# Kernel optimization log

Measured on AMD Instinct MI355X. Metric: run time of the kernel, lower is better.

The kernel has to match this reference:

```python
import jax, jax.numpy as jnp
import numpy as np

H = 256  # LSTM units == embedding dim

def _lstm(x, W, U, b):
    """Keras LSTM, return_sequences=True. x: [B,T,E] -> [B,T,H].
    Gate order i, f, g(c), o; sigmoid recurrent activation, tanh activation."""
    B = x.shape[0]
    xW = jnp.einsum('bte,eg->btg', x, W) + b  # [B,T,4H], input projection hoisted out of scan
    def step(carry, xw_t):
        h, c = carry
        z = xw_t + h @ U                      # [B,4H]
        i, f, g, o = jnp.split(z, 4, axis=-1)
        i = jax.nn.sigmoid(i); f = jax.nn.sigmoid(f)
        g = jnp.tanh(g);       o = jax.nn.sigmoid(o)
        c = f * c + i * g
        h = o * jnp.tanh(c)
        return (h, c), h
    h0 = jnp.zeros((B, H), x.dtype)
    (_, _), hs = jax.lax.scan(step, (h0, h0), jnp.swapaxes(xW, 0, 1))
    return jnp.swapaxes(hs, 0, 1)             # [B,T,H]

def _bilstm(x, Wf, Uf, bf, Wb, Ub, bb):
    fwd = _lstm(x, Wf, Uf, bf)
    bwd = _lstm(x[:, ::-1, :], Wb, Ub, bb)[:, ::-1, :]
    return jnp.concatenate([fwd, bwd], axis=-1)  # [B,T,2H]

def setup_inputs() -> dict:
    key = jax.random.key(0)
    ks = jax.random.split(key, 8)
    B, T, V, E = 256, 128, 32000, 256
    s = 0.05
    return {
        'tokens': jax.random.randint(ks[0], (B, T), 0, V, dtype=jnp.int32),
        'Emb': jax.random.normal(ks[1], (V, E), jnp.float32) * s,
        'Wf': jax.random.normal(ks[2], (3, E, 4 * H), jnp.float32) * s,
        'Uf': jax.random.normal(ks[3], (3, H, 4 * H), jnp.float32) * s,
        'bf': jnp.zeros((3, 4 * H), jnp.float32),
        'Wb': jax.random.normal(ks[4], (3, E, 4 * H), jnp.float32) * s,
        'Ub': jax.random.normal(ks[5], (3, H, 4 * H), jnp.float32) * s,
        'bb': jnp.zeros((3, 4 * H), jnp.float32),
    }

def reference(tokens, Emb, Wf, Uf, bf, Wb, Ub, bb):
    x = Emb[tokens]                             # [B,T,E]
    pools = []
    for l in range(3):                          # three parallel BiLSTM branches
        seq = _bilstm(x, Wf[l], Uf[l], bf[l], Wb[l], Ub[l], bb[l])  # [B,T,2H]
        pools.append(jnp.max(seq, axis=1))      # GlobalMaxPool1D -> [B,2H]
    return jnp.concatenate(pools, axis=1)       # [B,6H]
```

## Files before the change

### kernel.cpp

```cpp
#include <hip/hip_runtime.h>
#include <hip/hip_bf16.h>


#define NB 256
#define NT 128
#define NE 256
#define NH 256
#define NG 1024

using bf16x8 = __attribute__((ext_vector_type(8))) short;
using f32x4  = __attribute__((ext_vector_type(4))) float;
typedef unsigned long long u64;

#define X_OFF   0u
#define WT_OFF  16777216u
#define UT_OFF  19922944u
#define HB_OFF  23068672u
#define TAG_OFF 26214400u
#define HB_PAR_U64 196608

static __device__ __forceinline__ ushort f2bf(float f) {
  union { float f; unsigned u; } v; v.f = f;
  unsigned r = v.u + 0x7fffu + ((v.u >> 16) & 1u);
  return (ushort)(r >> 16);
}
static __device__ __forceinline__ float rcp_(float x) { return __builtin_amdgcn_rcpf(x); }
static __device__ __forceinline__ float sigf(float x) { return rcp_(1.f + __expf(-x)); }
static __device__ __forceinline__ float tanhf_(float x) { return 1.f - 2.f * rcp_(__expf(2.f * x) + 1.f); }

__global__ void k_embed(const int* __restrict__ tok, const float* __restrict__ emb,
                        ushort* __restrict__ x2) {
  const int tid = blockIdx.x * 256 + threadIdx.x;
  const int lane = tid & 63;
  const int nt = (tid >> 6) & 3;
  const int kt = (tid >> 8) & 7;
  const int bg = (tid >> 11) & 3;
  const int t  = tid >> 13;
  const int b  = bg * 64 + nt * 16 + (lane & 15);
  const int e0 = kt * 32 + (lane >> 4) * 8;
  const int tk = tok[b * NT + t];
  const float4 v0 = *(const float4*)(emb + (size_t)tk * NE + e0);
  const float4 v1 = *(const float4*)(emb + (size_t)tk * NE + e0 + 4);
  ushort4 o0, o1;
  o0.x = f2bf(v0.x); o0.y = f2bf(v0.y); o0.z = f2bf(v0.z); o0.w = f2bf(v0.w);
  o1.x = f2bf(v1.x); o1.y = f2bf(v1.y); o1.z = f2bf(v1.z); o1.w = f2bf(v1.w);
  ushort4* dst = (ushort4*)(x2 + (size_t)tid * 8);
  dst[0] = o0; dst[1] = o1;
}

__global__ void k_pack(const float* __restrict__ Wf, const float* __restrict__ Uf,
                       const float* __restrict__ Wb, const float* __restrict__ Ub,
                       ushort* __restrict__ wt, ushort* __restrict__ ut) {
  const int tid = blockIdx.x * 256 + threadIdx.x;
  const int l = tid & 63;
  const int mt = (tid >> 6) & 7;
  const int kt = (tid >> 9) & 7;
  const int cg = (tid >> 12) & 7;
  const int chain = tid >> 15;
  const int ll = chain >> 1, dir = chain & 1;
  const int ml = mt * 16 + (l & 15);
  const int hdl = ml >> 2, g = ml & 3;
  const int col = g * 256 + cg * 32 + hdl;
  const int k0 = kt * 32 + ((l >> 4) << 3);
  const float* W = (dir ? Wb : Wf) + (size_t)ll * NE * NG;
  const float* U = (dir ? Ub : Uf) + (size_t)ll * NH * NG;
  ushort vw[8], vu[8];
#pragma unroll
  for (int j = 0; j < 8; ++j) {
    vw[j] = f2bf(W[(size_t)(k0 + j) * NG + col]);
    vu[j] = f2bf(U[(size_t)(k0 + j) * NG + col]);
  }
  ushort4* dw = (ushort4*)(wt + (size_t)tid * 8);
  dw[0] = make_ushort4(vw[0], vw[1], vw[2], vw[3]);
  dw[1] = make_ushort4(vw[4], vw[5], vw[6], vw[7]);
  ushort4* du = (ushort4*)(ut + (size_t)tid * 8);
  du[0] = make_ushort4(vu[0], vu[1], vu[2], vu[3]);
  du[1] = make_ushort4(vu[4], vu[5], vu[6], vu[7]);
}

__global__ void k_init(uint* __restrict__ p) { p[threadIdx.x] = 0u; }

__global__ __launch_bounds__(512, 2) void k_lstm(
    const ushort* __restrict__ x2, const ushort* __restrict__ wt,
    const ushort* __restrict__ ut, const float* __restrict__ bf_,
    const float* __restrict__ bb_, ushort* __restrict__ hbuf,
    uint* __restrict__ tags, float* __restrict__ out) {
  __shared__ __align__(16) char smem[73728];

  const int bid = blockIdx.x;
  const int w = (bid & 7) * 24 + (bid >> 3);
  const int cg = w & 7, grp = w >> 3;
  const int chain = grp >> 2, bg = grp & 3;
  const int ll = chain >> 1, dir = chain & 1;
  const int tx = threadIdx.x;
  const int wv = tx >> 6, lane = tx & 63;
  const int mh = wv & 1, nt = wv >> 1;
  const int l15 = lane & 15, hi = lane >> 4;

  {
    const bf16x8* wsrc = (const bf16x8*)(wt + (size_t)(chain * 8 + cg) * 32768);
    bf16x8* wdst = (bf16x8*)smem;
#pragma unroll
    for (int i = 0; i < 8; ++i) wdst[i * 512 + tx] = wsrc[i * 512 + tx];
  }
  bf16x8 uf[8][4];
#pragma unroll
  for (int kt = 0; kt < 8; ++kt)
#pragma unroll
    for (int q = 0; q < 4; ++q)
      uf[kt][q] = *(const bf16x8*)(ut + ((size_t)((chain * 8 + cg) * 8 + kt) * 8 + mh * 4 + q) * 512 + lane * 8);

  const float* bias = (dir ? bb_ : bf_) + ll * NG;
  float bias_r[4][4];
#pragma unroll
  for (int q = 0; q < 4; ++q)
#pragma unroll
    for (int r = 0; r < 4; ++r)
      bias_r[q][r] = bias[r * 256 + cg * 32 + mh * 16 + q * 4 + hi];

  int pubaddr[4];
#pragma unroll
  for (int q = 0; q < 4; ++q) {
    const int lane2 = l15 | ((mh * 2 + (q >> 1)) << 4);
    const int slot = (q & 1) * 4 + hi;
    pubaddr[q] = 65536 + nt * 1024 + lane2 * 16 + slot * 2;
  }

  float c_[4] = {0.f, 0.f, 0.f, 0.f};
  float hm[4] = {-1e30f, -1e30f, -1e30f, -1e30f};

  uint* tag_own = tags + grp * 16 + cg;
  const uint* tag_poll = tags + grp * 16 + (lane & 7);
  u64* hb64 = (u64*)hbuf;
  __syncthreads();

  for (int tau = 0; tau < NT; ++tau) {
    const int t = dir ? (NT - 1 - tau) : tau;
    const ushort* xb_base = x2 + ((size_t)((t * 4 + bg) * 32 + nt)) * 512 + lane * 8;
    bf16x8 xb[8];
#pragma unroll
    for (int kt = 0; kt < 8; ++kt) xb[kt] = *(const bf16x8*)(xb_base + kt * 2048);

    f32x4 acc[4];
#pragma unroll
    for (int q = 0; q < 4; ++q)
      acc[q] = (f32x4){bias_r[q][0], bias_r[q][1], bias_r[q][2], bias_r[q][3]};

#pragma unroll
    for (int kt = 0; kt < 4; ++kt)
#pragma unroll
      for (int q = 0; q < 4; ++q) {
        const bf16x8 wA = *(const bf16x8*)(smem + ((kt * 8 + mh * 4 + q) * 64 + lane) * 16);
        acc[q] = __builtin_amdgcn_mfma_f32_16x16x32_bf16(wA, xb[kt], acc[q], 0, 0, 0);
      }

    if (tau > 0) {
      while (!__all(__hip_atomic_load(tag_poll, __ATOMIC_RELAXED, __HIP_MEMORY_SCOPE_AGENT) >= (uint)tau))
        __builtin_amdgcn_s_sleep(1);
      asm volatile("" ::: "memory");
    }

    u64 hq[16];
    if (tau > 0) {
      const u64* hs = hb64 + (size_t)((tau - 1) & 1) * HB_PAR_U64 + grp * 4096;
#pragma unroll
      for (int kt = 0; kt < 8; ++kt) {
        const int o = (kt * 4 + nt) * 128 + lane * 2;
        hq[kt * 2]     = __hip_atomic_load(hs + o,     __ATOMIC_RELAXED, __HIP_MEMORY_SCOPE_AGENT);
        hq[kt * 2 + 1] = __hip_atomic_load(hs + o + 1, __ATOMIC_RELAXED, __HIP_MEMORY_SCOPE_AGENT);
      }
    }

#pragma unroll
    for (int kt = 4; kt < 8; ++kt)
#pragma unroll
      for (int q = 0; q < 4; ++q) {
        const bf16x8 wA = *(const bf16x8*)(smem + ((kt * 8 + mh * 4 + q) * 64 + lane) * 16);
        acc[q] = __builtin_amdgcn_mfma_f32_16x16x32_bf16(wA, xb[kt], acc[q], 0, 0, 0);
      }

    if (tau > 0) {
#pragma unroll
      for (int kt = 0; kt < 8; ++kt) {
        union { u64 q[2]; bf16x8 v; } u;
        u.q[0] = hq[kt * 2]; u.q[1] = hq[kt * 2 + 1];
#pragma unroll
        for (int q = 0; q < 4; ++q)
          acc[q] = __builtin_amdgcn_mfma_f32_16x16x32_bf16(uf[kt][q], u.v, acc[q], 0, 0, 0);
      }
    }

    const int parb = (tau & 1) * 4096;
#pragma unroll
    for (int q = 0; q < 4; ++q) {
      const float iv = sigf(acc[q][0]);
      const float fv = sigf(acc[q][1]);
      const float gv = tanhf_(acc[q][2]);
      const float ov = sigf(acc[q][3]);
      const float cn = fv * c_[q] + iv * gv;
      c_[q] = cn;
      const float hv = ov * tanhf_(cn);
      hm[q] = fmaxf(hm[q], hv);
      *(ushort*)(smem + pubaddr[q] + parb) = f2bf(hv);
    }
    __syncthreads();

    if (tau + 1 < NT) {
      const u64 v = *(const u64*)(smem + 65536 + parb + tx * 8);
      __hip_atomic_store(hb64 + (size_t)(tau & 1) * HB_PAR_U64 + grp * 4096 + cg * 512 + tx,
                         v, __ATOMIC_RELAXED, __HIP_MEMORY_SCOPE_AGENT);
      asm volatile("s_waitcnt vmcnt(0)" ::: "memory");
      if (tx == 0)
        __hip_atomic_store(tag_own, (uint)(tau + 1), __ATOMIC_RELAXED, __HIP_MEMORY_SCOPE_AGENT);
    }
  }

#pragma unroll
  for (int q = 0; q < 4; ++q) {
    const int b = bg * 64 + nt * 16 + l15;
    const int col = ll * 512 + dir * 256 + cg * 32 + mh * 16 + q * 4 + hi;
    out[(size_t)b * 1536 + col] = hm[q];
  }
}

extern "C" void kernel_launch(void* const* d_in, const int* in_sizes, int n_in,
                              void* d_out, int out_size, void* d_ws, size_t ws_size,
                              hipStream_t stream) {
  (void)in_sizes; (void)n_in; (void)out_size; (void)ws_size;
  const int*   tokens = (const int*)d_in[0];
  const float* Emb    = (const float*)d_in[1];
  const float* Wf     = (const float*)d_in[2];
  const float* Uf     = (const float*)d_in[3];
  const float* bf_    = (const float*)d_in[4];
  const float* Wb     = (const float*)d_in[5];
  const float* Ub     = (const float*)d_in[6];
  const float* bb_    = (const float*)d_in[7];
  float* out = (float*)d_out;

  ushort* x2   = (ushort*)((char*)d_ws + X_OFF);
  ushort* wt   = (ushort*)((char*)d_ws + WT_OFF);
  ushort* ut   = (ushort*)((char*)d_ws + UT_OFF);
  ushort* hbuf = (ushort*)((char*)d_ws + HB_OFF);
  uint*   tags = (uint*)((char*)d_ws + TAG_OFF);

  hipLaunchKernelGGL(k_embed, dim3(4096), dim3(256), 0, stream, tokens, Emb, x2);
  hipLaunchKernelGGL(k_pack, dim3(768), dim3(256), 0, stream, Wf, Uf, Wb, Ub, wt, ut);
  hipLaunchKernelGGL(k_init, dim3(1), dim3(768), 0, stream, tags);
  hipLaunchKernelGGL(k_lstm, dim3(192), dim3(512), 0, stream, x2, wt, ut, bf_, bb_, hbuf, tags, out);
}
```

Measured before the change: 449.2 us.

## Pair forward and backward directions per block and pipeline hidden-state loads

Each block now runs both directions of one layer's column slice, with four waves per direction. Every wave covers all four batch tiles for two gate quads, so the grid halves to 96 blocks and each block holds both W slices in LDS. Hidden-state publishing now goes straight to global memory from each wave with per-wave tags, dropping the block-wide barrier and the LDS staging step. Polling is done by one wave per direction, which forwards readiness to the other waves through an LDS flag. The h loads are split into three batches interleaved with MFMAs to hide latency. In exchange, each block uses much more LDS and more registers, and the per-step publish now issues many scattered 2-byte atomic stores.

```diff
diff --git a/kernel.cpp b/kernel.cpp
--- a/kernel.cpp
+++ b/kernel.cpp
@@ -16,8 +16,9 @@
 #define WT_OFF  16777216u
 #define UT_OFF  19922944u
 #define HB_OFF  23068672u
-#define TAG_OFF 26214400u
-#define HB_PAR_U64 196608
+#define TAG_OFF 24641536u
+#define HB_PAR_U64 98304
+#define HB_PAR_US  393216
 
 static __device__ __forceinline__ ushort f2bf(float f) {
   union { float f; unsigned u; } v; v.f = f;
@@ -85,142 +86,208 @@
     const ushort* __restrict__ ut, const float* __restrict__ bf_,
     const float* __restrict__ bb_, ushort* __restrict__ hbuf,
     uint* __restrict__ tags, float* __restrict__ out) {
-  __shared__ __align__(16) char smem[73728];
+  __shared__ __align__(16) char smem[131200];
 
   const int bid = blockIdx.x;
-  const int w = (bid & 7) * 24 + (bid >> 3);
-  const int cg = w & 7, grp = w >> 3;
-  const int chain = grp >> 2, bg = grp & 3;
-  const int ll = chain >> 1, dir = chain & 1;
+  const int w = (bid & 7) * 12 + (bid >> 3);
+  const int ll = w >> 5, rr_ = w & 31, cg = rr_ >> 2, bg = rr_ & 3;
   const int tx = threadIdx.x;
   const int wv = tx >> 6, lane = tx & 63;
-  const int mh = wv & 1, nt = wv >> 1;
+  const int dir = wv >> 2, mq = wv & 3;
+  const int chain = ll * 2 + dir;
   const int l15 = lane & 15, hi = lane >> 4;
 
-  {
-    const bf16x8* wsrc = (const bf16x8*)(wt + (size_t)(chain * 8 + cg) * 32768);
-    bf16x8* wdst = (bf16x8*)smem;
+#pragma unroll
+  for (int d2 = 0; d2 < 2; ++d2) {
+    const bf16x8* wsrc = (const bf16x8*)(wt + (size_t)((ll * 2 + d2) * 8 + cg) * 32768);
+    bf16x8* wdst = (bf16x8*)(smem + d2 * 65536);
 #pragma unroll
     for (int i = 0; i < 8; ++i) wdst[i * 512 + tx] = wsrc[i * 512 + tx];
   }
-  bf16x8 uf[8][4];
+  bf16x8 uf[8][2];
 #pragma unroll
   for (int kt = 0; kt < 8; ++kt)
 #pragma unroll
-    for (int q = 0; q < 4; ++q)
-      uf[kt][q] = *(const bf16x8*)(ut + ((size_t)((chain * 8 + cg) * 8 + kt) * 8 + mh * 4 + q) * 512 + lane * 8);
+    for (int q = 0; q < 2; ++q)
+      uf[kt][q] = *(const bf16x8*)(ut + ((size_t)((chain * 8 + cg) * 8 + kt) * 8 + mq * 2 + q) * 512 + lane * 8);
 
   const float* bias = (dir ? bb_ : bf_) + ll * NG;
-  float bias_r[4][4];
-#pragma unroll
-  for (int q = 0; q < 4; ++q)
-#pragma unroll
-    for (int r = 0; r < 4; ++r)
-      bias_r[q][r] = bias[r * 256 + cg * 32 + mh * 16 + q * 4 + hi];
-
-  int pubaddr[4];
-#pragma unroll
-  for (int q = 0; q < 4; ++q) {
-    const int lane2 = l15 | ((mh * 2 + (q >> 1)) << 4);
-    const int slot = (q & 1) * 4 + hi;
-    pubaddr[q] = 65536 + nt * 1024 + lane2 * 16 + slot * 2;
-  }
-
-  float c_[4] = {0.f, 0.f, 0.f, 0.f};
-  float hm[4] = {-1e30f, -1e30f, -1e30f, -1e30f};
-
-  uint* tag_own = tags + grp * 16 + cg;
-  const uint* tag_poll = tags + grp * 16 + (lane & 7);
+  float bias_r[2][4];
+#pragma unroll
+  for (int q = 0; q < 2; ++q)
+#pragma unroll
+    for (int g = 0; g < 4; ++g)
+      bias_r[q][g] = bias[g * 256 + cg * 32 + mq * 8 + q * 4 + hi];
+
+  float c_[2][4], hm[2][4];
+#pragma unroll
+  for (int q = 0; q < 2; ++q)
+#pragma unroll
+    for (int nt = 0; nt < 4; ++nt) { c_[q][nt] = 0.f; hm[q][nt] = -1e30f; }
+
+  const int grpi = chain * 4 + bg;
+  uint* tag_base = tags + grpi * 32;
+  uint* tag_own  = tag_base + cg * 4 + mq;
+  const uint* tag_poll = tag_base + (lane & 31);
+  uint* lflag = (uint*)(smem + 131072 + dir * 64);
   u64* hb64 = (u64*)hbuf;
+  const size_t pslice_us = ((size_t)(grpi * 8 + cg) * 4 + mq) * 512;
+
+  if (tx < 2) *(volatile uint*)(smem + 131072 + tx * 64) = 0u;
   __syncthreads();
 
   for (int tau = 0; tau < NT; ++tau) {
     const int t = dir ? (NT - 1 - tau) : tau;
-    const ushort* xb_base = x2 + ((size_t)((t * 4 + bg) * 32 + nt)) * 512 + lane * 8;
-    bf16x8 xb[8];
-#pragma unroll
-    for (int kt = 0; kt < 8; ++kt) xb[kt] = *(const bf16x8*)(xb_base + kt * 2048);
-
-    f32x4 acc[4];
-#pragma unroll
-    for (int q = 0; q < 4; ++q)
-      acc[q] = (f32x4){bias_r[q][0], bias_r[q][1], bias_r[q][2], bias_r[q][3]};
-
-#pragma unroll
-    for (int kt = 0; kt < 4; ++kt)
-#pragma unroll
-      for (int q = 0; q < 4; ++q) {
-        const bf16x8 wA = *(const bf16x8*)(smem + ((kt * 8 + mh * 4 + q) * 64 + lane) * 16);
-        acc[q] = __builtin_amdgcn_mfma_f32_16x16x32_bf16(wA, xb[kt], acc[q], 0, 0, 0);
-      }
+    const ushort* xb_base = x2 + ((size_t)((t * 4 + bg) * 8) * 4) * 512;
+
+    f32x4 acc[2][4];
+#pragma unroll
+    for (int q = 0; q < 2; ++q)
+#pragma unroll
+      for (int nt = 0; nt < 4; ++nt)
+        acc[q][nt] = (f32x4){bias_r[q][0], bias_r[q][1], bias_r[q][2], bias_r[q][3]};
+
+#pragma unroll
+    for (int kt = 0; kt < 4; ++kt) {
+      bf16x8 xbv[4];
+#pragma unroll
+      for (int nt = 0; nt < 4; ++nt)
+        xbv[nt] = *(const bf16x8*)(xb_base + ((size_t)(kt * 4 + nt) * 64 + lane) * 8);
+#pragma unroll
+      for (int q = 0; q < 2; ++q) {
+        const bf16x8 wA = *(const bf16x8*)(smem + dir * 65536 + ((kt * 8 + mq * 2 + q) * 64 + lane) * 16);
+#pragma unroll
+        for (int nt = 0; nt < 4; ++nt)
+          acc[q][nt] = __builtin_amdgcn_mfma_f32_16x16x32_bf16(wA, xbv[nt], acc[q][nt], 0, 0, 0);
+      }
+    }
 
     if (tau > 0) {
-      while (!__all(__hip_atomic_load(tag_poll, __ATOMIC_RELAXED, __HIP_MEMORY_SCOPE_AGENT) >= (uint)tau))
-        __builtin_amdgcn_s_sleep(1);
+      if (mq == 0) {
+        while (!__all(__hip_atomic_load(tag_poll, __ATOMIC_RELAXED, __HIP_MEMORY_SCOPE_AGENT) >= (uint)tau))
+          __builtin_amdgcn_s_sleep(1);
+        if (lane == 0)
+          __hip_atomic_store(lflag, (uint)tau, __ATOMIC_RELAXED, __HIP_MEMORY_SCOPE_WORKGROUP);
+      } else {
+        while (__hip_atomic_load(lflag, __ATOMIC_RELAXED, __HIP_MEMORY_SCOPE_WORKGROUP) < (uint)tau)
+          __builtin_amdgcn_s_sleep(1);
+      }
       asm volatile("" ::: "memory");
     }
 
-    u64 hq[16];
+    u64 hqa[24], hqb[24], hqc[16];
+    const u64* hs = hb64 + (size_t)((tau - 1) & 1) * HB_PAR_U64;
     if (tau > 0) {
-      const u64* hs = hb64 + (size_t)((tau - 1) & 1) * HB_PAR_U64 + grp * 4096;
-#pragma unroll
-      for (int kt = 0; kt < 8; ++kt) {
-        const int o = (kt * 4 + nt) * 128 + lane * 2;
-        hq[kt * 2]     = __hip_atomic_load(hs + o,     __ATOMIC_RELAXED, __HIP_MEMORY_SCOPE_AGENT);
-        hq[kt * 2 + 1] = __hip_atomic_load(hs + o + 1, __ATOMIC_RELAXED, __HIP_MEMORY_SCOPE_AGENT);
-      }
-    }
-
-#pragma unroll
-    for (int kt = 4; kt < 8; ++kt)
-#pragma unroll
-      for (int q = 0; q < 4; ++q) {
-        const bf16x8 wA = *(const bf16x8*)(smem + ((kt * 8 + mh * 4 + q) * 64 + lane) * 16);
-        acc[q] = __builtin_amdgcn_mfma_f32_16x16x32_bf16(wA, xb[kt], acc[q], 0, 0, 0);
-      }
+#pragma unroll
+      for (int kt = 0; kt < 3; ++kt) {
+        const u64* sp = hs + ((size_t)(grpi * 8 + kt) * 4 + hi) * 128 + l15 * 2;
+#pragma unroll
+        for (int nt = 0; nt < 4; ++nt) {
+          hqa[kt * 8 + nt * 2]     = __hip_atomic_load(sp + nt * 32,     __ATOMIC_RELAXED, __HIP_MEMORY_SCOPE_AGENT);
+          hqa[kt * 8 + nt * 2 + 1] = __hip_atomic_load(sp + nt * 32 + 1, __ATOMIC_RELAXED, __HIP_MEMORY_SCOPE_AGENT);
+        }
+      }
+    }
+
+#pragma unroll
+    for (int kt = 4; kt < 8; ++kt) {
+      bf16x8 xbv[4];
+#pragma unroll
+      for (int nt = 0; nt < 4; ++nt)
+        xbv[nt] = *(const bf16x8*)(xb_base + ((size_t)(kt * 4 + nt) * 64 + lane) * 8);
+#pragma unroll
+      for (int q = 0; q < 2; ++q) {
+        const bf16x8 wA = *(const bf16x8*)(smem + dir * 65536 + ((kt * 8 + mq * 2 + q) * 64 + lane) * 16);
+#pragma unroll
+        for (int nt = 0; nt < 4; ++nt)
+          acc[q][nt] = __builtin_amdgcn_mfma_f32_16x16x32_bf16(wA, xbv[nt], acc[q][nt], 0, 0, 0);
+      }
+    }
 
     if (tau > 0) {
 #pragma unroll
-      for (int kt = 0; kt < 8; ++kt) {
-        union { u64 q[2]; bf16x8 v; } u;
-        u.q[0] = hq[kt * 2]; u.q[1] = hq[kt * 2 + 1];
-#pragma unroll
-        for (int q = 0; q < 4; ++q)
-          acc[q] = __builtin_amdgcn_mfma_f32_16x16x32_bf16(uf[kt][q], u.v, acc[q], 0, 0, 0);
-      }
-    }
-
-    const int parb = (tau & 1) * 4096;
-#pragma unroll
-    for (int q = 0; q < 4; ++q) {
-      const float iv = sigf(acc[q][0]);
-      const float fv = sigf(acc[q][1]);
-      const float gv = tanhf_(acc[q][2]);
-      const float ov = sigf(acc[q][3]);
-      const float cn = fv * c_[q] + iv * gv;
-      c_[q] = cn;
-      const float hv = ov * tanhf_(cn);
-      hm[q] = fmaxf(hm[q], hv);
-      *(ushort*)(smem + pubaddr[q] + parb) = f2bf(hv);
-    }
-    __syncthreads();
-
-    if (tau + 1 < NT) {
-      const u64 v = *(const u64*)(smem + 65536 + parb + tx * 8);
-      __hip_atomic_store(hb64 + (size_t)(tau & 1) * HB_PAR_U64 + grp * 4096 + cg * 512 + tx,
-                         v, __ATOMIC_RELAXED, __HIP_MEMORY_SCOPE_AGENT);
+      for (int kt = 3; kt < 6; ++kt) {
+        const u64* sp = hs + ((size_t)(grpi * 8 + kt) * 4 + hi) * 128 + l15 * 2;
+#pragma unroll
+        for (int nt = 0; nt < 4; ++nt) {
+          hqb[(kt - 3) * 8 + nt * 2]     = __hip_atomic_load(sp + nt * 32,     __ATOMIC_RELAXED, __HIP_MEMORY_SCOPE_AGENT);
+          hqb[(kt - 3) * 8 + nt * 2 + 1] = __hip_atomic_load(sp + nt * 32 + 1, __ATOMIC_RELAXED, __HIP_MEMORY_SCOPE_AGENT);
+        }
+      }
+#pragma unroll
+      for (int kt = 0; kt < 3; ++kt)
+#pragma unroll
+        for (int nt = 0; nt < 4; ++nt) {
+          union { u64 qq[2]; bf16x8 v; } u;
+          u.qq[0] = hqa[kt * 8 + nt * 2]; u.qq[1] = hqa[kt * 8 + nt * 2 + 1];
+#pragma unroll
+          for (int q = 0; q < 2; ++q)
+            acc[q][nt] = __builtin_amdgcn_mfma_f32_16x16x32_bf16(uf[kt][q], u.v, acc[q][nt], 0, 0, 0);
+        }
+#pragma unroll
+      for (int kt = 6; kt < 8; ++kt) {
+        const u64* sp = hs + ((size_t)(grpi * 8 + kt) * 4 + hi) * 128 + l15 * 2;
+#pragma unroll
+        for (int nt = 0; nt < 4; ++nt) {
+          hqc[(kt - 6) * 8 + nt * 2]     = __hip_atomic_load(sp + nt * 32,     __ATOMIC_RELAXED, __HIP_MEMORY_SCOPE_AGENT);
+          hqc[(kt - 6) * 8 + nt * 2 + 1] = __hip_atomic_load(sp + nt * 32 + 1, __ATOMIC_RELAXED, __HIP_MEMORY_SCOPE_AGENT);
+        }
+      }
+#pragma unroll
+      for (int kt = 3; kt < 6; ++kt)
+#pragma unroll
+        for (int nt = 0; nt < 4; ++nt) {
+          union { u64 qq[2]; bf16x8 v; } u;
+          u.qq[0] = hqb[(kt - 3) * 8 + nt * 2]; u.qq[1] = hqb[(kt - 3) * 8 + nt * 2 + 1];
+#pragma unroll
+          for (int q = 0; q < 2; ++q)
+            acc[q][nt] = __builtin_amdgcn_mfma_f32_16x16x32_bf16(uf[kt][q], u.v, acc[q][nt], 0, 0, 0);
+        }
+#pragma unroll
+      for (int kt = 6; kt < 8; ++kt)
+#pragma unroll
+        for (int nt = 0; nt < 4; ++nt) {
+          union { u64 qq[2]; bf16x8 v; } u;
+          u.qq[0] = hqc[(kt - 6) * 8 + nt * 2]; u.qq[1] = hqc[(kt - 6) * 8 + nt * 2 + 1];
+#pragma unroll
+          for (int q = 0; q < 2; ++q)
+            acc[q][nt] = __builtin_amdgcn_mfma_f32_16x16x32_bf16(uf[kt][q], u.v, acc[q][nt], 0, 0, 0);
+        }
+    }
+
+    ushort* pw = hbuf + (size_t)(tau & 1) * HB_PAR_US + pslice_us;
+    const bool dopub = (tau + 1 < NT);
+#pragma unroll
+    for (int q = 0; q < 2; ++q)
+#pragma unroll
+      for (int nt = 0; nt < 4; ++nt) {
+        const float iv = sigf(acc[q][nt][0]);
+        const float fv = sigf(acc[q][nt][1]);
+        const float gv = tanhf_(acc[q][nt][2]);
+        const float ov = sigf(acc[q][nt][3]);
+        const float cn = fv * c_[q][nt] + iv * gv;
+        c_[q][nt] = cn;
+        const float hv = ov * tanhf_(cn);
+        hm[q][nt] = fmaxf(hm[q][nt], hv);
+        if (dopub)
+          __hip_atomic_store(pw + nt * 128 + l15 * 8 + q * 4 + hi, f2bf(hv),
+                             __ATOMIC_RELAXED, __HIP_MEMORY_SCOPE_AGENT);
+      }
+    if (dopub) {
       asm volatile("s_waitcnt vmcnt(0)" ::: "memory");
-      if (tx == 0)
+      if (lane == 0)
         __hip_atomic_store(tag_own, (uint)(tau + 1), __ATOMIC_RELAXED, __HIP_MEMORY_SCOPE_AGENT);
     }
   }
 
 #pragma unroll
-  for (int q = 0; q < 4; ++q) {
-    const int b = bg * 64 + nt * 16 + l15;
-    const int col = ll * 512 + dir * 256 + cg * 32 + mh * 16 + q * 4 + hi;
-    out[(size_t)b * 1536 + col] = hm[q];
-  }
+  for (int q = 0; q < 2; ++q)
+#pragma unroll
+    for (int nt = 0; nt < 4; ++nt) {
+      const int b = bg * 64 + nt * 16 + l15;
+      const int col = ll * 512 + dir * 256 + cg * 32 + mq * 8 + q * 4 + hi;
+      out[(size_t)b * 1536 + col] = hm[q][nt];
+    }
 }
 
 extern "C" void kernel_launch(void* const* d_in, const int* in_sizes, int n_in,
@@ -246,5 +313,5 @@
   hipLaunchKernelGGL(k_embed, dim3(4096), dim3(256), 0, stream, tokens, Emb, x2);
   hipLaunchKernelGGL(k_pack, dim3(768), dim3(256), 0, stream, Wf, Uf, Wb, Ub, wt, ut);
   hipLaunchKernelGGL(k_init, dim3(1), dim3(768), 0, stream, tags);
-  hipLaunchKernelGGL(k_lstm, dim3(192), dim3(512), 0, stream, x2, wt, ut, bf_, bb_, hbuf, tags, out);
-}
+  hipLaunchKernelGGL(k_lstm, dim3(96), dim3(512), 0, stream, x2, wt, ut, bf_, bb_, hbuf, tags, out);
+}
```

Measured after the change: 1.196 ms. 166% more time.
